# Performance work log

Hardware: AMD Instinct MI355X
Metric: run time of the kernel (lower is better)

## Reference

```python
import jax, jax.numpy as jnp
import numpy as np

B, T, D, E, I = 4, 2048, 2048, 8, 1024
TOP_K = 2
AUX_COEFF = 0.01


def setup_inputs() -> dict:
    key = jax.random.key(0)
    kx, kg, k1, k3, k2 = jax.random.split(key, 5)
    scale = 0.02
    x = jax.random.normal(kx, (B, T, D), dtype=jnp.float32)
    gate_w = jax.random.normal(kg, (E, D), dtype=jnp.float32) * scale   # nn.Linear weight [out,in]
    w1 = jax.random.normal(k1, (E, I, D), dtype=jnp.float32) * scale    # gate_proj per expert
    w3 = jax.random.normal(k3, (E, I, D), dtype=jnp.float32) * scale    # up_proj per expert
    w2 = jax.random.normal(k2, (E, D, I), dtype=jnp.float32) * scale    # down_proj per expert
    return {"x": x, "gate_w": gate_w, "w1": w1, "w3": w3, "w2": w2}


def reference(x, gate_w, w1, w3, w2):
    b, t, d = x.shape
    e = gate_w.shape[0]
    xf = x.reshape(b * t, d)                                   # [N, D]
    logits = xf @ gate_w.T                                     # [N, E]
    scores = jax.nn.softmax(logits, axis=-1)
    top_scores, top_idx = jax.lax.top_k(scores, TOP_K)         # [N, K]
    top_scores = top_scores / jnp.sum(top_scores, axis=-1, keepdims=True)
    # load-balancing aux loss (Switch Transformer)
    expert_mask = jax.nn.one_hot(top_idx, e, dtype=x.dtype).sum(axis=1)  # [N, E]
    f = expert_mask.mean(axis=0)
    p = scores.mean(axis=0)
    aux_loss = AUX_COEFF * e * jnp.sum(f * p)
    # dense all-expert SwiGLU (matches torch module's dense dispatch)
    h = jax.nn.silu(jnp.einsum('td,eid->tei', xf, w1)) * jnp.einsum('td,eid->tei', xf, w3)  # [N,E,I]
    expert_outs = jnp.einsum('tei,edi->ted', h, w2)            # [N, E, D]
    selected = jnp.take_along_axis(expert_outs, top_idx[:, :, None], axis=1)  # [N, K, D]
    out = jnp.sum(selected * top_scores[:, :, None], axis=1)   # [N, D]
    return out.reshape(b, t, d), aux_loss
```

## Files before the change

kernel.cpp:

```cpp
#include <hip/hip_runtime.h>
#include <hip/hip_bf16.h>

constexpr int kN = 8192;
constexpr int kD = 2048;
constexpr int kE = 8;
constexpr int kI = 1024;

typedef __bf16 bf16x8 __attribute__((ext_vector_type(8)));
typedef float  f32x16 __attribute__((ext_vector_type(16)));

constexpr size_t OFF_COUNTS = 0;
constexpr size_t OFF_PSUM   = 64;
constexpr size_t OFF_OFFS   = 128;
constexpr size_t OFF_CURSOR = 192;
constexpr size_t OFF_TBASE  = 256;
constexpr size_t OFF_TOPE   = 320;
constexpr size_t OFF_TOPW   = OFF_TOPE + (size_t)kN * 8;
constexpr size_t OFF_SLOT   = OFF_TOPW + (size_t)kN * 8;
constexpr size_t OFF_TOK    = OFF_SLOT + (size_t)kN * 8;
constexpr size_t OFF_XG     = OFF_TOK + (size_t)kN * 8 + 64;
constexpr size_t OFF_W1B    = OFF_XG  + (size_t)2 * kN * kD * 2;
constexpr size_t OFF_W3B    = OFF_W1B + (size_t)kE * kI * kD * 2;
constexpr size_t OFF_W2B    = OFF_W3B + (size_t)kE * kI * kD * 2;
constexpr size_t OFF_H      = OFF_W2B + (size_t)kE * kD * kI * 2;
constexpr size_t OFF_O2     = OFF_XG;

typedef __attribute__((address_space(1))) const unsigned GU;
typedef __attribute__((address_space(3))) unsigned LU;
__device__ __forceinline__ void gload16(const void* g, void* l) {
    __builtin_amdgcn_global_load_lds((GU*)g, (LU*)l, 16, 0, 0);
}

constexpr int kMaxTiles = 136;
constexpr int kGemmGrid = kMaxTiles * 16;

__global__ __launch_bounds__(256) void convert3_kernel(
    const float* __restrict__ s0, const float* __restrict__ s1,
    const float* __restrict__ s2,
    __bf16* __restrict__ d0, __bf16* __restrict__ d1, __bf16* __restrict__ d2,
    int n8seg)
{
    const int seg = blockIdx.x >> 11;
    const int bid = blockIdx.x & 2047;
    const float* src = (seg == 0) ? s0 : (seg == 1) ? s1 : s2;
    __bf16*      dst = (seg == 0) ? d0 : (seg == 1) ? d1 : d2;
    int i = bid * 256 + threadIdx.x;
    const int stride = 2048 * 256;
    for (; i < n8seg; i += stride) {
        const float4* s = (const float4*)(src + (size_t)i * 8);
        float4 f0 = s[0], f1 = s[1];
        bf16x8 v;
        v[0]=(__bf16)f0.x; v[1]=(__bf16)f0.y; v[2]=(__bf16)f0.z; v[3]=(__bf16)f0.w;
        v[4]=(__bf16)f1.x; v[5]=(__bf16)f1.y; v[6]=(__bf16)f1.z; v[7]=(__bf16)f1.w;
        *(bf16x8*)(dst + (size_t)i * 8) = v;
    }
}

__global__ __launch_bounds__(256) void gate_kernel(
    const float* __restrict__ x, const float* __restrict__ gw,
    unsigned* __restrict__ counts, float* __restrict__ psum,
    int2* __restrict__ tope, float2* __restrict__ topw)
{
    const int tid  = threadIdx.x;
    const int lane = tid & 63;
    const int wv   = tid >> 6;
    const int t    = blockIdx.x * 4 + wv;

    const float* xr = x + (size_t)t * kD;
    float xv[32];
#pragma unroll
    for (int j = 0; j < 32; ++j) xv[j] = xr[lane + 64 * j];

    float s[8];
#pragma unroll
    for (int e = 0; e < 8; ++e) {
        const float* gr = gw + (size_t)e * kD;
        float a = 0.f;
#pragma unroll
        for (int j = 0; j < 32; ++j) a += xv[j] * gr[lane + 64 * j];
        s[e] = a;
    }
#pragma unroll
    for (int off = 32; off > 0; off >>= 1) {
#pragma unroll
        for (int e = 0; e < 8; ++e) s[e] += __shfl_xor(s[e], off, 64);
    }
    float mx = s[0];
#pragma unroll
    for (int e = 1; e < 8; ++e) mx = fmaxf(mx, s[e]);
    float p[8]; float sum = 0.f;
#pragma unroll
    for (int e = 0; e < 8; ++e) { p[e] = expf(s[e] - mx); sum += p[e]; }
    float inv = 1.f / sum;
#pragma unroll
    for (int e = 0; e < 8; ++e) p[e] *= inv;

    int e0 = 0; float p0 = p[0];
#pragma unroll
    for (int e = 1; e < 8; ++e) if (p[e] > p0) { p0 = p[e]; e0 = e; }
    int e1 = -1; float p1 = -1.f;
#pragma unroll
    for (int e = 0; e < 8; ++e) if (e != e0 && p[e] > p1) { p1 = p[e]; e1 = e; }
    float wn = 1.f / (p0 + p1);

    __shared__ float ps[4][8];
    __shared__ unsigned cnt[8];
    if (tid < 8) cnt[tid] = 0u;
    __syncthreads();
    if (lane == 0) {
#pragma unroll
        for (int e = 0; e < 8; ++e) ps[wv][e] = p[e];
        atomicAdd(&cnt[e0], 1u);
        atomicAdd(&cnt[e1], 1u);
        tope[t] = make_int2(e0, e1);
        topw[t] = make_float2(p0 * wn, p1 * wn);
    }
    __syncthreads();
    if (tid < 8) {
        atomicAdd(&psum[tid], ps[0][tid] + ps[1][tid] + ps[2][tid] + ps[3][tid]);
        if (cnt[tid]) atomicAdd(&counts[tid], cnt[tid]);
    }
}

__global__ void scan_kernel(const unsigned* __restrict__ counts,
                            const float* __restrict__ psum,
                            unsigned* __restrict__ offs,
                            unsigned* __restrict__ cursor,
                            unsigned* __restrict__ tbase,
                            float* __restrict__ out)
{
    if (threadIdx.x == 0) {
        unsigned off = 0, tb = 0;
        float a = 0.f;
        for (int e = 0; e < 8; ++e) {
            offs[e] = off; cursor[e] = off; off += counts[e];
            tbase[e] = tb; tb += (counts[e] + 127u) >> 7;
            a += ((float)counts[e] / (float)kN) * (psum[e] / (float)kN);
        }
        tbase[8] = tb;
        out[(size_t)kN * kD] = 0.01f * (float)kE * a;
    }
}

__global__ __launch_bounds__(256) void scatter_kernel(
    const int2* __restrict__ tope,
    unsigned* __restrict__ cursor, int* __restrict__ tok,
    int2* __restrict__ slotmap)
{
    int t = blockIdx.x * 256 + threadIdx.x;
    int2 ee = tope[t];
    unsigned q0 = atomicAdd(&cursor[ee.x], 1u);
    tok[q0] = t;
    unsigned q1 = atomicAdd(&cursor[ee.y], 1u);
    tok[q1] = t;
    slotmap[t] = make_int2((int)q0, (int)q1);
}

__global__ __launch_bounds__(256) void gather_kernel(
    const float* __restrict__ x, const int* __restrict__ tok,
    __bf16* __restrict__ Xg)
{
    const int total = 2 * kN * (kD / 8);
    int i = blockIdx.x * 256 + threadIdx.x;
    const int stride = gridDim.x * 256;
    for (; i < total; i += stride) {
        const int slot = i >> 8;
        const int d8   = (i & 255) * 8;
        const float4* s = (const float4*)(x + (size_t)tok[slot] * kD + d8);
        float4 f0 = s[0], f1 = s[1];
        bf16x8 v;
        v[0]=(__bf16)f0.x; v[1]=(__bf16)f0.y; v[2]=(__bf16)f0.z; v[3]=(__bf16)f0.w;
        v[4]=(__bf16)f1.x; v[5]=(__bf16)f1.y; v[6]=(__bf16)f1.z; v[7]=(__bf16)f1.w;
        *(bf16x8*)(Xg + (size_t)slot * kD + d8) = v;
    }
}

__device__ __forceinline__ bool gemm_decode(
    const unsigned* __restrict__ tbase, int& e, int& mt, int& ct)
{
    const unsigned w = blockIdx.x;
    const unsigned orig = (w & 7u) * (kGemmGrid / 8) + (w >> 3);
    const int tile = (int)(orig >> 4);
    ct = (int)(orig & 15u);
    if ((unsigned)tile >= tbase[8]) return false;
    e = 0;
#pragma unroll
    for (int k = 1; k < 8; ++k) if (tbase[k] <= (unsigned)tile) e = k;
    mt = tile - (int)tbase[e];
    return true;
}

__global__ __launch_bounds__(256) void ffn_h_kernel(
    const __bf16* __restrict__ Xg,
    const __bf16* __restrict__ w1b, const __bf16* __restrict__ w3b,
    const unsigned* __restrict__ counts, const unsigned* __restrict__ offs,
    const unsigned* __restrict__ tbase, __bf16* __restrict__ H)
{
    int e, mt, ct;
    if (!gemm_decode(tbase, e, mt, ct)) return;
    const unsigned n_e = counts[e];
    const unsigned base = offs[e];

    __shared__ __bf16 As[128][64];
    __shared__ __bf16 Bs[128][64];

    const int tid  = threadIdx.x;
    const int lane = tid & 63;
    const int wv   = tid >> 6;
    const int wr   = wv >> 1, wc = wv & 1;

    const __bf16* aptr[4];
    const __bf16* bptr[4];
    __bf16* alds[4];
    __bf16* blds[4];
#pragma unroll
    for (int j = 0; j < 4; ++j) {
        const int r = wv * 32 + j * 8 + (lane >> 3);
        const int c = (((lane & 7) ^ (r & 7)) << 3);
        unsigned grow = (unsigned)(mt * 128 + r);
        grow = grow < n_e ? grow : (n_e - 1);
        aptr[j] = Xg + (size_t)(base + grow) * kD + c;
        alds[j] = &As[wv * 32 + j * 8][0];
        const int rr = r & 63;
        const int h  = ct * 64 + ((r >> 6) << 5) + (rr & 31);
        const __bf16* wsrc = (rr < 32) ? w1b : w3b;
        bptr[j] = wsrc + ((size_t)e * kI + h) * kD + c;
        blds[j] = &Bs[wv * 32 + j * 8][0];
    }

    f32x16 acc[2][2] = {};

    const int ar0 = wr * 64 + (lane & 31);
    const int ar1 = ar0 + 32;
    const int br0 = wc * 64 + (lane & 31);
    const int br1 = br0 + 32;
    const int sgl = lane >> 5;

    for (int k0 = 0; k0 < kD; k0 += 64) {
#pragma unroll
        for (int j = 0; j < 4; ++j) {
            gload16(aptr[j], alds[j]);
            gload16(bptr[j], blds[j]);
            aptr[j] += 64; bptr[j] += 64;
        }
        __syncthreads();

#pragma unroll
        for (int kk = 0; kk < 4; ++kk) {
            const int s = kk * 2 + sgl;
            bf16x8 a0 = *(const bf16x8*)&As[ar0][((s ^ (ar0 & 7)) << 3)];
            bf16x8 a1 = *(const bf16x8*)&As[ar1][((s ^ (ar1 & 7)) << 3)];
            bf16x8 b0 = *(const bf16x8*)&Bs[br0][((s ^ (br0 & 7)) << 3)];
            bf16x8 b1 = *(const bf16x8*)&Bs[br1][((s ^ (br1 & 7)) << 3)];
            acc[0][0] = __builtin_amdgcn_mfma_f32_32x32x16_bf16(a0, b0, acc[0][0], 0, 0, 0);
            acc[0][1] = __builtin_amdgcn_mfma_f32_32x32x16_bf16(a0, b1, acc[0][1], 0, 0, 0);
            acc[1][0] = __builtin_amdgcn_mfma_f32_32x32x16_bf16(a1, b0, acc[1][0], 0, 0, 0);
            acc[1][1] = __builtin_amdgcn_mfma_f32_32x32x16_bf16(a1, b1, acc[1][1], 0, 0, 0);
        }
        __syncthreads();
    }

    const int c0    = lane & 31;
    const int rbase = 4 * (lane >> 5);
    const size_t hcol = (size_t)(ct * 64 + wc * 32 + c0);
#pragma unroll
    for (int m = 0; m < 2; ++m) {
#pragma unroll
        for (int reg = 0; reg < 16; ++reg) {
            const int crow = (reg & 3) + 8 * (reg >> 2) + rbase;
            const unsigned grow = (unsigned)(mt * 128 + wr * 64 + m * 32 + crow);
            if (grow < n_e) {
                float a1 = acc[m][0][reg];
                float a3 = acc[m][1][reg];
                float h = a1 / (1.f + __expf(-a1)) * a3;
                H[(size_t)(base + grow) * kI + hcol] = (__bf16)h;
            }
        }
    }
}

__global__ __launch_bounds__(256) void ffn_out_kernel(
    const __bf16* __restrict__ H, const __bf16* __restrict__ w2b,
    const unsigned* __restrict__ counts, const unsigned* __restrict__ offs,
    const unsigned* __restrict__ tbase, __bf16* __restrict__ O2)
{
    int e, mt, ct;
    if (!gemm_decode(tbase, e, mt, ct)) return;
    const unsigned n_e = counts[e];
    const unsigned base = offs[e];

    __shared__ __bf16 As[128][64];
    __shared__ __bf16 Bs[128][64];

    const int tid  = threadIdx.x;
    const int lane = tid & 63;
    const int wv   = tid >> 6;
    const int wr   = wv >> 1, wc = wv & 1;

    const __bf16* aptr[4];
    const __bf16* bptr[4];
    __bf16* alds[4];
    __bf16* blds[4];
#pragma unroll
    for (int j = 0; j < 4; ++j) {
        const int r = wv * 32 + j * 8 + (lane >> 3);
        const int c = (((lane & 7) ^ (r & 7)) << 3);
        unsigned grow = (unsigned)(mt * 128 + r);
        grow = grow < n_e ? grow : (n_e - 1);
        aptr[j] = H + (size_t)(base + grow) * kI + c;
        alds[j] = &As[wv * 32 + j * 8][0];
        bptr[j] = w2b + ((size_t)e * kD + ct * 128 + r) * kI + c;
        blds[j] = &Bs[wv * 32 + j * 8][0];
    }

    f32x16 acc[2][2] = {};

    const int ar0 = wr * 64 + (lane & 31);
    const int ar1 = ar0 + 32;
    const int br0 = wc * 64 + (lane & 31);
    const int br1 = br0 + 32;
    const int sgl = lane >> 5;

    for (int k0 = 0; k0 < kI; k0 += 64) {
#pragma unroll
        for (int j = 0; j < 4; ++j) {
            gload16(aptr[j], alds[j]);
            gload16(bptr[j], blds[j]);
            aptr[j] += 64; bptr[j] += 64;
        }
        __syncthreads();

#pragma unroll
        for (int kk = 0; kk < 4; ++kk) {
            const int s = kk * 2 + sgl;
            bf16x8 a0 = *(const bf16x8*)&As[ar0][((s ^ (ar0 & 7)) << 3)];
            bf16x8 a1 = *(const bf16x8*)&As[ar1][((s ^ (ar1 & 7)) << 3)];
            bf16x8 b0 = *(const bf16x8*)&Bs[br0][((s ^ (br0 & 7)) << 3)];
            bf16x8 b1 = *(const bf16x8*)&Bs[br1][((s ^ (br1 & 7)) << 3)];
            acc[0][0] = __builtin_amdgcn_mfma_f32_32x32x16_bf16(a0, b0, acc[0][0], 0, 0, 0);
            acc[0][1] = __builtin_amdgcn_mfma_f32_32x32x16_bf16(a0, b1, acc[0][1], 0, 0, 0);
            acc[1][0] = __builtin_amdgcn_mfma_f32_32x32x16_bf16(a1, b0, acc[1][0], 0, 0, 0);
            acc[1][1] = __builtin_amdgcn_mfma_f32_32x32x16_bf16(a1, b1, acc[1][1], 0, 0, 0);
        }
        __syncthreads();
    }

    const int c0    = lane & 31;
    const int rbase = 4 * (lane >> 5);
#pragma unroll
    for (int m = 0; m < 2; ++m) {
#pragma unroll
        for (int reg = 0; reg < 16; ++reg) {
            const int crow = (reg & 3) + 8 * (reg >> 2) + rbase;
            const unsigned grow = (unsigned)(mt * 128 + wr * 64 + m * 32 + crow);
            if (grow < n_e) {
                __bf16* orow = O2 + (size_t)(base + grow) * kD + ct * 128 + wc * 64 + c0;
                orow[0]  = (__bf16)acc[m][0][reg];
                orow[32] = (__bf16)acc[m][1][reg];
            }
        }
    }
}

__global__ __launch_bounds__(256) void combine_kernel(
    const __bf16* __restrict__ O2, const int2* __restrict__ slotmap,
    const float2* __restrict__ topw, float* __restrict__ out)
{
    const int total = kN * (kD / 8);
    int i = blockIdx.x * 256 + threadIdx.x;
    const int stride = gridDim.x * 256;
    for (; i < total; i += stride) {
        const int t  = i >> 8;
        const int d8 = (i & 255) * 8;
        const int2   sm = slotmap[t];
        const float2 w  = topw[t];
        bf16x8 a = *(const bf16x8*)(O2 + (size_t)sm.x * kD + d8);
        bf16x8 b = *(const bf16x8*)(O2 + (size_t)sm.y * kD + d8);
        float r[8];
#pragma unroll
        for (int j = 0; j < 8; ++j)
            r[j] = w.x * (float)a[j] + w.y * (float)b[j];
        float4* o = (float4*)(out + (size_t)i * 8);
        o[0] = make_float4(r[0], r[1], r[2], r[3]);
        o[1] = make_float4(r[4], r[5], r[6], r[7]);
    }
}

extern "C" void kernel_launch(void* const* d_in, const int* in_sizes, int n_in,
                              void* d_out, int out_size, void* d_ws, size_t ws_size,
                              hipStream_t stream)
{
    const float* x  = (const float*)d_in[0];
    const float* gw = (const float*)d_in[1];
    const float* w1 = (const float*)d_in[2];
    const float* w3 = (const float*)d_in[3];
    const float* w2 = (const float*)d_in[4];
    float* out = (float*)d_out;
    char*  ws  = (char*)d_ws;

    unsigned* counts = (unsigned*)(ws + OFF_COUNTS);
    float*    psum   = (float*)(ws + OFF_PSUM);
    unsigned* offs   = (unsigned*)(ws + OFF_OFFS);
    unsigned* cursor = (unsigned*)(ws + OFF_CURSOR);
    unsigned* tbase  = (unsigned*)(ws + OFF_TBASE);
    int2*     tope   = (int2*)(ws + OFF_TOPE);
    float2*   topw   = (float2*)(ws + OFF_TOPW);
    int2*     slotmap= (int2*)(ws + OFF_SLOT);
    int*      tok    = (int*)(ws + OFF_TOK);
    __bf16*   Xg     = (__bf16*)(ws + OFF_XG);
    __bf16*   w1b    = (__bf16*)(ws + OFF_W1B);
    __bf16*   w3b    = (__bf16*)(ws + OFF_W3B);
    __bf16*   w2b    = (__bf16*)(ws + OFF_W2B);
    __bf16*   H      = (__bf16*)(ws + OFF_H);
    __bf16*   O2     = (__bf16*)(ws + OFF_O2);

    hipMemsetAsync(d_ws, 0, 320, stream);

    gate_kernel<<<kN / 4, 256, 0, stream>>>(x, gw, counts, psum, tope, topw);
    scan_kernel<<<1, 64, 0, stream>>>(counts, psum, offs, cursor, tbase, out);
    scatter_kernel<<<kN / 256, 256, 0, stream>>>(tope, cursor, tok, slotmap);

    convert3_kernel<<<3 * 2048, 256, 0, stream>>>(
        w1, w3, w2, w1b, w3b, w2b, kE * kI * kD / 8);
    gather_kernel<<<2048, 256, 0, stream>>>(x, tok, Xg);

    ffn_h_kernel<<<kGemmGrid, 256, 0, stream>>>(
        Xg, w1b, w3b, counts, offs, tbase, H);
    ffn_out_kernel<<<kGemmGrid, 256, 0, stream>>>(
        H, w2b, counts, offs, tbase, O2);
    combine_kernel<<<2048, 256, 0, stream>>>(O2, slotmap, topw, out);
}
```

Measured before the change: 460.6 us.

## Fuse x bf16 conversion into gate kernel and gather rows inside ffn_h

The gate kernel now also writes a bf16 copy of x, and its loads become float2 vectors. The separate gather kernel, which built a duplicated 2N-row bf16 activation buffer, is removed. ffn_h now loads token indices for its 128-row tile into shared memory and reads A rows from the bf16 x copy indirectly. O2 is moved to alias the w1b/w3b region, which is safe because those weights are dead by the time the output GEMM writes. This cuts a full read of fp32 x for two slots per token plus a large bf16 write, at the cost of non-contiguous row addresses in the first GEMM's A loads and an extra sync at kernel start.

After: 486.4 us. 5.6% more time.

```diff
diff --git a/kernel.cpp b/kernel.cpp
--- a/kernel.cpp
+++ b/kernel.cpp
@@ -18,12 +18,12 @@
 constexpr size_t OFF_TOPW   = OFF_TOPE + (size_t)kN * 8;
 constexpr size_t OFF_SLOT   = OFF_TOPW + (size_t)kN * 8;
 constexpr size_t OFF_TOK    = OFF_SLOT + (size_t)kN * 8;
-constexpr size_t OFF_XG     = OFF_TOK + (size_t)kN * 8 + 64;
-constexpr size_t OFF_W1B    = OFF_XG  + (size_t)2 * kN * kD * 2;
+constexpr size_t OFF_XB     = OFF_TOK + (size_t)kN * 8 + 64;
+constexpr size_t OFF_W1B    = OFF_XB  + (size_t)kN * kD * 2;
 constexpr size_t OFF_W3B    = OFF_W1B + (size_t)kE * kI * kD * 2;
 constexpr size_t OFF_W2B    = OFF_W3B + (size_t)kE * kI * kD * 2;
 constexpr size_t OFF_H      = OFF_W2B + (size_t)kE * kD * kI * 2;
-constexpr size_t OFF_O2     = OFF_XG;
+constexpr size_t OFF_O2     = OFF_W1B;
 
 typedef __attribute__((address_space(1))) const unsigned GU;
 typedef __attribute__((address_space(3))) unsigned LU;
@@ -59,25 +59,38 @@
 __global__ __launch_bounds__(256) void gate_kernel(
     const float* __restrict__ x, const float* __restrict__ gw,
     unsigned* __restrict__ counts, float* __restrict__ psum,
-    int2* __restrict__ tope, float2* __restrict__ topw)
+    int2* __restrict__ tope, float2* __restrict__ topw,
+    __bf16* __restrict__ xb)
 {
     const int tid  = threadIdx.x;
     const int lane = tid & 63;
     const int wv   = tid >> 6;
     const int t    = blockIdx.x * 4 + wv;
 
-    const float* xr = x + (size_t)t * kD;
-    float xv[32];
-#pragma unroll
-    for (int j = 0; j < 32; ++j) xv[j] = xr[lane + 64 * j];
+    const float2* xr = (const float2*)(x + (size_t)t * kD);
+    float2 xv[16];
+#pragma unroll
+    for (int j = 0; j < 16; ++j) xv[j] = xr[lane + 64 * j];
+
+    unsigned* xbr = (unsigned*)(xb + (size_t)t * kD);
+#pragma unroll
+    for (int j = 0; j < 16; ++j) {
+        union { __bf16 h[2]; unsigned u; } p;
+        p.h[0] = (__bf16)xv[j].x;
+        p.h[1] = (__bf16)xv[j].y;
+        xbr[lane + 64 * j] = p.u;
+    }
 
     float s[8];
 #pragma unroll
     for (int e = 0; e < 8; ++e) {
-        const float* gr = gw + (size_t)e * kD;
+        const float2* gr = (const float2*)(gw + (size_t)e * kD);
         float a = 0.f;
 #pragma unroll
-        for (int j = 0; j < 32; ++j) a += xv[j] * gr[lane + 64 * j];
+        for (int j = 0; j < 16; ++j) {
+            float2 g = gr[lane + 64 * j];
+            a += xv[j].x * g.x + xv[j].y * g.y;
+        }
         s[e] = a;
     }
 #pragma unroll
@@ -156,25 +169,6 @@
     slotmap[t] = make_int2((int)q0, (int)q1);
 }
 
-__global__ __launch_bounds__(256) void gather_kernel(
-    const float* __restrict__ x, const int* __restrict__ tok,
-    __bf16* __restrict__ Xg)
-{
-    const int total = 2 * kN * (kD / 8);
-    int i = blockIdx.x * 256 + threadIdx.x;
-    const int stride = gridDim.x * 256;
-    for (; i < total; i += stride) {
-        const int slot = i >> 8;
-        const int d8   = (i & 255) * 8;
-        const float4* s = (const float4*)(x + (size_t)tok[slot] * kD + d8);
-        float4 f0 = s[0], f1 = s[1];
-        bf16x8 v;
-        v[0]=(__bf16)f0.x; v[1]=(__bf16)f0.y; v[2]=(__bf16)f0.z; v[3]=(__bf16)f0.w;
-        v[4]=(__bf16)f1.x; v[5]=(__bf16)f1.y; v[6]=(__bf16)f1.z; v[7]=(__bf16)f1.w;
-        *(bf16x8*)(Xg + (size_t)slot * kD + d8) = v;
-    }
-}
-
 __device__ __forceinline__ bool gemm_decode(
     const unsigned* __restrict__ tbase, int& e, int& mt, int& ct)
 {
@@ -191,10 +185,11 @@
 }
 
 __global__ __launch_bounds__(256) void ffn_h_kernel(
-    const __bf16* __restrict__ Xg,
+    const __bf16* __restrict__ xb,
     const __bf16* __restrict__ w1b, const __bf16* __restrict__ w3b,
     const unsigned* __restrict__ counts, const unsigned* __restrict__ offs,
-    const unsigned* __restrict__ tbase, __bf16* __restrict__ H)
+    const unsigned* __restrict__ tbase, const int* __restrict__ tok,
+    __bf16* __restrict__ H)
 {
     int e, mt, ct;
     if (!gemm_decode(tbase, e, mt, ct)) return;
@@ -203,29 +198,30 @@
 
     __shared__ __bf16 As[128][64];
     __shared__ __bf16 Bs[128][64];
+    __shared__ int rowtok[128];
 
     const int tid  = threadIdx.x;
     const int lane = tid & 63;
     const int wv   = tid >> 6;
     const int wr   = wv >> 1, wc = wv & 1;
 
+    if (tid < 128) {
+        unsigned r = (unsigned)(mt * 128 + tid);
+        rowtok[tid] = tok[base + (r < n_e ? r : (n_e - 1))];
+    }
+    __syncthreads();
+
     const __bf16* aptr[4];
     const __bf16* bptr[4];
-    __bf16* alds[4];
-    __bf16* blds[4];
 #pragma unroll
     for (int j = 0; j < 4; ++j) {
         const int r = wv * 32 + j * 8 + (lane >> 3);
         const int c = (((lane & 7) ^ (r & 7)) << 3);
-        unsigned grow = (unsigned)(mt * 128 + r);
-        grow = grow < n_e ? grow : (n_e - 1);
-        aptr[j] = Xg + (size_t)(base + grow) * kD + c;
-        alds[j] = &As[wv * 32 + j * 8][0];
+        aptr[j] = xb + (size_t)rowtok[r] * kD + c;
         const int rr = r & 63;
         const int h  = ct * 64 + ((r >> 6) << 5) + (rr & 31);
         const __bf16* wsrc = (rr < 32) ? w1b : w3b;
         bptr[j] = wsrc + ((size_t)e * kI + h) * kD + c;
-        blds[j] = &Bs[wv * 32 + j * 8][0];
     }
 
     f32x16 acc[2][2] = {};
@@ -239,8 +235,8 @@
     for (int k0 = 0; k0 < kD; k0 += 64) {
 #pragma unroll
         for (int j = 0; j < 4; ++j) {
-            gload16(aptr[j], alds[j]);
-            gload16(bptr[j], blds[j]);
+            gload16(aptr[j], &As[wv * 32 + j * 8][0]);
+            gload16(bptr[j], &Bs[wv * 32 + j * 8][0]);
             aptr[j] += 64; bptr[j] += 64;
         }
         __syncthreads();
@@ -299,8 +295,6 @@
 
     const __bf16* aptr[4];
     const __bf16* bptr[4];
-    __bf16* alds[4];
-    __bf16* blds[4];
 #pragma unroll
     for (int j = 0; j < 4; ++j) {
         const int r = wv * 32 + j * 8 + (lane >> 3);
@@ -308,9 +302,7 @@
         unsigned grow = (unsigned)(mt * 128 + r);
         grow = grow < n_e ? grow : (n_e - 1);
         aptr[j] = H + (size_t)(base + grow) * kI + c;
-        alds[j] = &As[wv * 32 + j * 8][0];
         bptr[j] = w2b + ((size_t)e * kD + ct * 128 + r) * kI + c;
-        blds[j] = &Bs[wv * 32 + j * 8][0];
     }
 
     f32x16 acc[2][2] = {};
@@ -324,8 +316,8 @@
     for (int k0 = 0; k0 < kI; k0 += 64) {
 #pragma unroll
         for (int j = 0; j < 4; ++j) {
-            gload16(aptr[j], alds[j]);
-            gload16(bptr[j], blds[j]);
+            gload16(aptr[j], &As[wv * 32 + j * 8][0]);
+            gload16(bptr[j], &Bs[wv * 32 + j * 8][0]);
             aptr[j] += 64; bptr[j] += 64;
         }
         __syncthreads();
@@ -407,7 +399,7 @@
     float2*   topw   = (float2*)(ws + OFF_TOPW);
     int2*     slotmap= (int2*)(ws + OFF_SLOT);
     int*      tok    = (int*)(ws + OFF_TOK);
-    __bf16*   Xg     = (__bf16*)(ws + OFF_XG);
+    __bf16*   xb     = (__bf16*)(ws + OFF_XB);
     __bf16*   w1b    = (__bf16*)(ws + OFF_W1B);
     __bf16*   w3b    = (__bf16*)(ws + OFF_W3B);
     __bf16*   w2b    = (__bf16*)(ws + OFF_W2B);
@@ -416,16 +408,15 @@
 
     hipMemsetAsync(d_ws, 0, 320, stream);
 
-    gate_kernel<<<kN / 4, 256, 0, stream>>>(x, gw, counts, psum, tope, topw);
+    gate_kernel<<<kN / 4, 256, 0, stream>>>(x, gw, counts, psum, tope, topw, xb);
     scan_kernel<<<1, 64, 0, stream>>>(counts, psum, offs, cursor, tbase, out);
     scatter_kernel<<<kN / 256, 256, 0, stream>>>(tope, cursor, tok, slotmap);
 
     convert3_kernel<<<3 * 2048, 256, 0, stream>>>(
         w1, w3, w2, w1b, w3b, w2b, kE * kI * kD / 8);
-    gather_kernel<<<2048, 256, 0, stream>>>(x, tok, Xg);
 
     ffn_h_kernel<<<kGemmGrid, 256, 0, stream>>>(
-        Xg, w1b, w3b, counts, offs, tbase, H);
+        xb, w1b, w3b, counts, offs, tbase, tok, H);
     ffn_out_kernel<<<kGemmGrid, 256, 0, stream>>>(
         H, w2b, counts, offs, tbase, O2);
     combine_kernel<<<2048, 256, 0, stream>>>(O2, slotmap, topw, out);
```
